# Kernel optimization log

Hardware: AMD Instinct MI355X
Metric: run time of the kernel (lower is better)

The kernel has to match this reference:

```python
import jax, jax.numpy as jnp
import numpy as np

N_EMBD = 1024
N_HEAD = 16
HEAD_DIM = N_EMBD // N_HEAD  # 64
KV_RANK = 256
Q_RANK = 512
ROPE_DIM = 32
B, T = 2, 2048
EPS = 1e-6


def _rope_tables(T, dim):
    inv_freq = 1.0 / (10000.0 ** (np.arange(0, dim, 2, dtype=np.float32) / dim))
    t = np.arange(T, dtype=np.float32)
    freqs = np.outer(t, inv_freq)            # [T, dim/2]
    emb = np.concatenate([freqs, freqs], -1)  # [T, dim]
    return jnp.asarray(np.cos(emb)), jnp.asarray(np.sin(emb))


def _apply_rope(x, cos, sin):
    # x: [B, H, T, D]; cos/sin: [T, D]
    d2 = x.shape[-1] // 2
    x1, x2 = x[..., :d2], x[..., d2:]
    rot = jnp.concatenate([-x2, x1], axis=-1)
    return x * cos[None, None, :, :] + rot * sin[None, None, :, :]


def setup_inputs() -> dict:
    key = jax.random.key(0)
    ks = jax.random.split(key, 10)
    def w(k, fan_in, fan_out):
        return jax.random.normal(k, (fan_in, fan_out), dtype=jnp.float32) * (fan_in ** -0.5)
    return {
        "x": jax.random.normal(ks[0], (B, T, N_EMBD), dtype=jnp.float32),
        "W_kv": w(ks[1], N_EMBD, KV_RANK),
        "g_kv": jnp.ones((KV_RANK,), dtype=jnp.float32),
        "W_kdec": w(ks[2], KV_RANK, N_HEAD * HEAD_DIM),
        "W_vdec": w(ks[3], KV_RANK, N_HEAD * HEAD_DIM),
        "W_q": w(ks[4], N_EMBD, Q_RANK),
        "W_qdec": w(ks[5], Q_RANK, N_HEAD * HEAD_DIM),
        "W_krope": w(ks[6], N_EMBD, N_HEAD * ROPE_DIM),
        "W_qrope": w(ks[7], Q_RANK, N_HEAD * ROPE_DIM),
        "W_o": w(ks[8], N_HEAD * HEAD_DIM, N_EMBD),
    }


def reference(x, W_kv, g_kv, W_kdec, W_vdec, W_q, W_qdec, W_krope, W_qrope, W_o):
    Bx, Tx, C = x.shape
    # low-rank compression
    kv_c = x @ W_kv                                    # [B,T,R_kv]
    kv_c = kv_c * jax.lax.rsqrt(jnp.mean(kv_c * kv_c, axis=-1, keepdims=True) + EPS) * g_kv
    q_c = x @ W_q                                       # [B,T,R_q]
    # decompress to per-head content / rope parts -> [B,H,T,D]
    def heads(y, d):
        return y.reshape(Bx, Tx, N_HEAD, d).transpose(0, 2, 1, 3)
    k_content = heads(kv_c @ W_kdec, HEAD_DIM)
    v = heads(kv_c @ W_vdec, HEAD_DIM)
    q_content = heads(q_c @ W_qdec, HEAD_DIM)
    k_rope = heads(x @ W_krope, ROPE_DIM)
    q_rope = heads(q_c @ W_qrope, ROPE_DIM)
    cos, sin = _rope_tables(Tx, ROPE_DIM)
    q_rope = _apply_rope(q_rope, cos, sin)
    k_rope = _apply_rope(k_rope, cos, sin)
    q = jnp.concatenate([q_content, q_rope], axis=-1)   # [B,H,T,D+Dr]
    k = jnp.concatenate([k_content, k_rope], axis=-1)
    scale = 1.0 / jnp.sqrt(jnp.float32(q.shape[-1]))
    scores = jnp.einsum('bhqd,bhkd->bhqk', q, k) * scale  # [B,H,T,T]
    causal = jnp.tril(jnp.ones((Tx, Tx), dtype=bool))
    scores = jnp.where(causal[None, None], scores, jnp.float32(-jnp.inf))
    attn = jax.nn.softmax(scores, axis=-1)
    out = jnp.einsum('bhqk,bhkd->bhqd', attn, v)          # [B,H,T,D]
    out = out.transpose(0, 2, 1, 3).reshape(Bx, Tx, N_HEAD * HEAD_DIM)
    return out @ W_o
```

## Files before the change

### kernel.cpp

```cpp
#include <hip/hip_runtime.h>
#include <hip/hip_bf16.h>
#include <math.h>

#define Bz 2
#define Tz 2048
#define Cz 1024
#define Hz 16
#define Dz 64
#define Rz 32
#define KVR 256
#define QR 512
#define DQK 96
#define Mz (Bz*Tz)
#define BHT (Bz*Hz*Tz)
#define QK_SCALE 0.10206207261596577f
#define QK_SCALE2 0.14724538519399733f
#define THR2 11.541560327111707f

typedef __attribute__((ext_vector_type(8))) short short8;
typedef __attribute__((ext_vector_type(4))) float f32x4;
typedef __attribute__((ext_vector_type(4))) unsigned short ushort4v;

__device__ __forceinline__ unsigned short f2bf(float f) {
    union { float f; unsigned u; } un; un.f = f;
    unsigned r = un.u + 0x7FFF + ((un.u >> 16) & 1);
    return (unsigned short)(r >> 16);
}

__device__ __forceinline__ void gload_lds16(const void* g, void* l) {
    __builtin_amdgcn_global_load_lds(
        (const __attribute__((address_space(1))) unsigned int*)g,
        (__attribute__((address_space(3))) unsigned int*)l, 16, 0, 0);
}

__global__ __launch_bounds__(256) void conv_f32_bf16(const float* __restrict__ in,
                                                     unsigned short* __restrict__ out,
                                                     int n)
{
    int i = (blockIdx.x * 256 + threadIdx.x) * 4;
    if (i >= n) return;
    float4 v = *(const float4*)&in[i];
    ushort4v o = { f2bf(v.x), f2bf(v.y), f2bf(v.z), f2bf(v.w) };
    *(ushort4v*)&out[i] = o;
}

struct TDesc8 {
    const float* src[8];
    unsigned short* dst[8];
    int K[8], N[8];
    int tile0[9];
};

__global__ __launch_bounds__(256) void transpose_all(TDesc8 p)
{
    __shared__ float ts[32][33];
    int t = blockIdx.x;
    int wi = 0;
    #pragma unroll
    for (int i = 0; i < 7; i++) if (t >= p.tile0[i + 1]) wi = i + 1;
    int lt = t - p.tile0[wi];
    int K = p.K[wi], N = p.N[wi];
    int kT = K >> 5;
    int k0 = (lt % kT) * 32, n0 = (lt / kT) * 32;
    const float* in = p.src[wi];
    unsigned short* out = p.dst[wi];

    int tid = threadIdx.x;
    int r = tid >> 5, cc = tid & 31;
    #pragma unroll
    for (int l = 0; l < 4; l++)
        ts[r + l * 8][cc] = in[(size_t)(k0 + r + l * 8) * N + n0 + cc];
    __syncthreads();
    #pragma unroll
    for (int l = 0; l < 4; l++)
        out[(size_t)(n0 + r + l * 8) * K + k0 + cc] = f2bf(ts[cc][r + l * 8]);
}

template<int EMODE>
__global__ __launch_bounds__(64) void gemm1w(
    const unsigned short* __restrict__ A, const unsigned short* __restrict__ Wt,
    void* __restrict__ O0, void* __restrict__ O1, void* __restrict__ O2,
    int K, float scale)
{
    __shared__ __attribute__((aligned(16))) unsigned short As[64 * 64];
    __shared__ __attribute__((aligned(16))) unsigned short Bs[64 * 64];

    const int lane = threadIdx.x;
    const int c = lane & 15, g = lane >> 4;
    const int m0 = blockIdx.x * 64, n0 = blockIdx.y * 64;
    const int rl = lane >> 3, c8 = lane & 7;

    f32x4 acc[4][4] = {};

    auto stage = [&](int k0) {
        if (EMODE == 4) {
            int h = k0 >> 6;
            #pragma unroll
            for (int i = 0; i < 8; i++) {
                int m = m0 + i * 8 + rl;
                int b = m >> 11, t = m & (Tz - 1);
                gload_lds16(&A[(((size_t)b * Hz + h) * Tz + t) * 64 + c8 * 8],
                            &As[(i * 64 + lane) * 8]);
            }
        } else {
            #pragma unroll
            for (int i = 0; i < 8; i++)
                gload_lds16(&A[(size_t)(m0 + i * 8 + rl) * K + k0 + c8 * 8],
                            &As[(i * 64 + lane) * 8]);
        }
        #pragma unroll
        for (int i = 0; i < 8; i++)
            gload_lds16(&Wt[(size_t)(n0 + i * 8 + rl) * K + k0 + c8 * 8],
                        &Bs[(i * 64 + lane) * 8]);
    };

    stage(0);

    for (int k0 = 0; k0 < K; k0 += 64) {
        asm volatile("s_waitcnt vmcnt(0)" ::: "memory");
        __builtin_amdgcn_sched_barrier(0);

        short8 af[2][4], bfr[2][4];
        #pragma unroll
        for (int ks = 0; ks < 2; ks++) {
            #pragma unroll
            for (int mq = 0; mq < 4; mq++)
                af[ks][mq] = *(const short8*)&As[(mq * 16 + c) * 64 + ks * 32 + g * 8];
            #pragma unroll
            for (int nt = 0; nt < 4; nt++)
                bfr[ks][nt] = *(const short8*)&Bs[(nt * 16 + c) * 64 + ks * 32 + g * 8];
        }
        asm volatile("s_waitcnt lgkmcnt(0)" ::: "memory");
        __builtin_amdgcn_sched_barrier(0);

        if (k0 + 64 < K) stage(k0 + 64);

        __builtin_amdgcn_s_setprio(1);
        #pragma unroll
        for (int ks = 0; ks < 2; ks++)
            #pragma unroll
            for (int mq = 0; mq < 4; mq++)
                #pragma unroll
                for (int nt = 0; nt < 4; nt++)
                    acc[mq][nt] = __builtin_amdgcn_mfma_f32_16x16x32_bf16(
                        af[ks][mq], bfr[ks][nt], acc[mq][nt], 0, 0, 0);
        __builtin_amdgcn_s_setprio(0);
    }

    #pragma unroll
    for (int mq = 0; mq < 4; mq++) {
        #pragma unroll
        for (int r = 0; r < 4; r++) {
            int m = m0 + mq * 16 + g * 4 + r;
            int b = m >> 11, t = m & (Tz - 1);

            if (EMODE == 1) {
                if (n0 < 256) {
                    #pragma unroll
                    for (int nt = 0; nt < 4; nt++)
                        ((float*)O0)[(size_t)m * 256 + n0 + nt * 16 + c] = acc[mq][nt][r];
                } else if (n0 < 768) {
                    #pragma unroll
                    for (int nt = 0; nt < 4; nt++)
                        ((unsigned short*)O1)[(size_t)m * 512 + (n0 - 256) + nt * 16 + c] =
                            f2bf(acc[mq][nt][r]);
                } else {
                    float inv = __expf(-(float)c * 0.5756462732485114f);
                    float ang = (float)t * inv;
                    float cs = cosf(ang), sn = sinf(ang);
                    #pragma unroll
                    for (int np = 0; np < 4; np += 2) {
                        float v0 = acc[mq][np][r];
                        float v1 = acc[mq][np + 1][r];
                        int col0 = (n0 - 768) + np * 16;
                        int h = col0 >> 5;
                        size_t base = (((size_t)b * Hz + h) * Tz + t) * DQK + 64;
                        ((unsigned short*)O2)[base + c]      = f2bf(v0 * cs - v1 * sn);
                        ((unsigned short*)O2)[base + c + 16] = f2bf(v1 * cs + v0 * sn);
                    }
                }
            } else if (EMODE == 2) {
                if (n0 < 1024) {
                    #pragma unroll
                    for (int nt = 0; nt < 4; nt++) {
                        int n = n0 + nt * 16 + c;
                        int h = n >> 6, dd = n & 63;
                        ((unsigned short*)O0)[(((size_t)b * Hz + h) * Tz + t) * DQK + dd] =
                            f2bf(acc[mq][nt][r] * scale);
                    }
                } else {
                    float inv = __expf(-(float)c * 0.5756462732485114f);
                    float ang = (float)t * inv;
                    float cs = cosf(ang), sn = sinf(ang);
                    #pragma unroll
                    for (int np = 0; np < 4; np += 2) {
                        float v0 = acc[mq][np][r] * scale;
                        float v1 = acc[mq][np + 1][r] * scale;
                        int col0 = (n0 - 1024) + np * 16;
                        int h = col0 >> 5;
                        size_t base = (((size_t)b * Hz + h) * Tz + t) * DQK + 64;
                        ((unsigned short*)O0)[base + c]      = f2bf(v0 * cs - v1 * sn);
                        ((unsigned short*)O0)[base + c + 16] = f2bf(v1 * cs + v0 * sn);
                    }
                }
            } else if (EMODE == 3) {
                if (n0 < 1024) {
                    #pragma unroll
                    for (int nt = 0; nt < 4; nt++) {
                        int n = n0 + nt * 16 + c;
                        int h = n >> 6, dd = n & 63;
                        ((unsigned short*)O0)[(((size_t)b * Hz + h) * Tz + t) * DQK + dd] =
                            f2bf(acc[mq][nt][r]);
                    }
                } else {
                    #pragma unroll
                    for (int nt = 0; nt < 4; nt++) {
                        int n = (n0 - 1024) + nt * 16 + c;
                        int h = n >> 6, dd = n & 63;
                        ((unsigned short*)O1)[(((size_t)b * Hz + h) * 64 + dd) * Tz + t] =
                            f2bf(acc[mq][nt][r]);
                    }
                }
            } else {
                #pragma unroll
                for (int nt = 0; nt < 4; nt++)
                    ((float*)O0)[(size_t)m * 1024 + n0 + nt * 16 + c] = acc[mq][nt][r];
            }
        }
    }
}

__global__ __launch_bounds__(256) void rmsnorm_k(const float* __restrict__ kv,
                                                 const float* __restrict__ g,
                                                 unsigned short* __restrict__ outb)
{
    int row = blockIdx.x * 4 + (threadIdx.x >> 6);
    int lane = threadIdx.x & 63;
    const float* p = kv + (size_t)row * 256;
    float v[4];
    float ss = 0.f;
    #pragma unroll
    for (int i = 0; i < 4; i++) { v[i] = p[lane + i * 64]; ss += v[i] * v[i]; }
    #pragma unroll
    for (int o = 32; o > 0; o >>= 1) ss += __shfl_xor(ss, o);
    float r = rsqrtf(ss * (1.f / 256.f) + 1e-6f);
    #pragma unroll
    for (int i = 0; i < 4; i++)
        outb[(size_t)row * 256 + lane + i * 64] = f2bf(v[i] * r * g[lane + i * 64]);
}

#define PSTR 72

__global__ __launch_bounds__(256, 3) void attn_mfma(
    const unsigned short* __restrict__ q,
    const unsigned short* __restrict__ k,
    const unsigned short* __restrict__ vt,
    unsigned short* __restrict__ o)
{
    __shared__ __attribute__((aligned(16))) unsigned short Ks[64 * 96];
    __shared__ __attribute__((aligned(16))) unsigned short Ps[4][16 * PSTR];

    int tid = threadIdx.x;
    int lane = tid & 63;
    int w = tid >> 6;
    int c = lane & 15, g = lane >> 4;

    int s = blockIdx.x;
    int bh = s & 31;
    int j = s >> 5;
    int qt = (j < 16) ? (31 - j) : (j - 16);
    int q0 = qt * 64;
    int ntiles = qt + 1;

    const unsigned short* qb = q + (size_t)bh * Tz * DQK;
    const unsigned short* kb = k + (size_t)bh * Tz * DQK;
    const unsigned short* vb = vt + (size_t)bh * 64 * Tz;
    unsigned short* ps = &Ps[w][0];

    int soff[3], sidx[3];
    #pragma unroll
    for (int i = 0; i < 3; i++) {
        int id2 = tid + i * 256;
        int srow = id2 / 12, sc8 = id2 % 12;
        soff[i] = srow * DQK + sc8 * 8;
        sidx[i] = (srow * 96 + sc8 * 8) ^ ((srow & 7) << 3);
    }

    short8 qf[3];
    {
        const unsigned short* qrow = qb + (size_t)(q0 + w * 16 + c) * DQK;
        #pragma unroll
        for (int kc = 0; kc < 3; kc++)
            qf[kc] = *(const short8*)(qrow + kc * 32 + g * 8);
    }

    short8 kreg[3];
    #pragma unroll
    for (int i = 0; i < 3; i++)
        kreg[i] = *(const short8*)&kb[soff[i]];
    #pragma unroll
    for (int i = 0; i < 3; i++)
        *(short8*)&Ks[sidx[i]] = kreg[i];
    __syncthreads();

    f32x4 oacc[4] = {};
    float mrun = -1e30f, lrun = 0.f;

    for (int t = 0; t < ntiles; t++) {
        int kt0 = t * 64;
        bool more = (t + 1) < ntiles;

        if (more) {
            #pragma unroll
            for (int i = 0; i < 3; i++)
                kreg[i] = *(const short8*)&kb[(size_t)(kt0 + 64) * DQK + soff[i]];
        }
        short8 vf[2][4];
        #pragma unroll
        for (int kc2 = 0; kc2 < 2; kc2++)
            #pragma unroll
            for (int nt = 0; nt < 4; nt++)
                vf[kc2][nt] = *(const short8*)&vb[(size_t)(nt * 16 + c) * Tz + kt0 + kc2 * 32 + g * 8];

        f32x4 sacc[4] = {};
        __builtin_amdgcn_s_setprio(1);
        #pragma unroll
        for (int kc = 0; kc < 3; kc++) {
            #pragma unroll
            for (int nt = 0; nt < 4; nt++) {
                short8 kf = *(const short8*)&Ks[((nt * 16 + c) * 96 + kc * 32 + g * 8) ^ ((c & 7) << 3)];
                sacc[nt] = __builtin_amdgcn_mfma_f32_16x16x32_bf16(kf, qf[kc], sacc[nt], 0, 0, 0);
            }
        }
        __builtin_amdgcn_s_setprio(0);

        __syncthreads();
        if (more) {
            #pragma unroll
            for (int i = 0; i < 3; i++)
                *(short8*)&Ks[sidx[i]] = kreg[i];
        }

        if (kt0 == q0) {
            #pragma unroll
            for (int nt = 0; nt < 4; nt++)
                #pragma unroll
                for (int r = 0; r < 4; r++)
                    if (nt * 16 + g * 4 + r > w * 16 + c)
                        sacc[nt][r] = -1e30f;
        }

        float pm = sacc[0][0];
        #pragma unroll
        for (int nt = 0; nt < 4; nt++)
            #pragma unroll
            for (int r = 0; r < 4; r++)
                pm = fmaxf(pm, sacc[nt][r]);
        pm = fmaxf(pm, __shfl_xor(pm, 16));
        pm = fmaxf(pm, __shfl_xor(pm, 32));

        bool need = pm > mrun + THR2;
        if (__ballot(need)) {
            float mn = fmaxf(mrun, pm);
            float sc = exp2f(mrun - mn);
            mrun = mn;
            float rs = 0.f;
            #pragma unroll
            for (int nt = 0; nt < 4; nt++)
                #pragma unroll
                for (int r = 0; r < 4; r++) {
                    sacc[nt][r] = exp2f(sacc[nt][r] - mrun);
                    rs += sacc[nt][r];
                }
            rs += __shfl_xor(rs, 16);
            rs += __shfl_xor(rs, 32);
            lrun = lrun * sc + rs;
            float scr[4];
            #pragma unroll
            for (int r = 0; r < 4; r++) scr[r] = __shfl(sc, g * 4 + r);
            #pragma unroll
            for (int nt = 0; nt < 4; nt++)
                #pragma unroll
                for (int r = 0; r < 4; r++)
                    oacc[nt][r] *= scr[r];
        } else {
            float rs = 0.f;
            #pragma unroll
            for (int nt = 0; nt < 4; nt++)
                #pragma unroll
                for (int r = 0; r < 4; r++) {
                    sacc[nt][r] = exp2f(sacc[nt][r] - mrun);
                    rs += sacc[nt][r];
                }
            rs += __shfl_xor(rs, 16);
            rs += __shfl_xor(rs, 32);
            lrun += rs;
        }

        #pragma unroll
        for (int nt = 0; nt < 4; nt++)
            #pragma unroll
            for (int rp = 0; rp < 2; rp++) {
                unsigned w32;
                asm("v_cvt_pk_bf16_f32 %0, %1, %2"
                    : "=v"(w32) : "v"(sacc[nt][2 * rp]), "v"(sacc[nt][2 * rp + 1]));
                *(unsigned*)&ps[c * PSTR + nt * 16 + g * 4 + 2 * rp] = w32;
            }
        __builtin_amdgcn_wave_barrier();

        __builtin_amdgcn_s_setprio(1);
        #pragma unroll
        for (int kc2 = 0; kc2 < 2; kc2++) {
            short8 pf = *(const short8*)&ps[c * PSTR + kc2 * 32 + g * 8];
            #pragma unroll
            for (int nt = 0; nt < 4; nt++)
                oacc[nt] = __builtin_amdgcn_mfma_f32_16x16x32_bf16(pf, vf[kc2][nt], oacc[nt], 0, 0, 0);
        }
        __builtin_amdgcn_s_setprio(0);
        __builtin_amdgcn_wave_barrier();

        __syncthreads();
    }

    float lr[4];
    #pragma unroll
    for (int r = 0; r < 4; r++) lr[r] = __shfl(lrun, g * 4 + r);
    #pragma unroll
    for (int nt = 0; nt < 4; nt++)
        #pragma unroll
        for (int r = 0; r < 4; r++)
            o[((size_t)bh * Tz + q0 + w * 16 + g * 4 + r) * 64 + nt * 16 + c] =
                f2bf(oacc[nt][r] / lr[r]);
}

extern "C" void kernel_launch(void* const* d_in, const int* in_sizes, int n_in,
                              void* d_out, int out_size, void* d_ws, size_t ws_size,
                              hipStream_t stream)
{
    const float* x       = (const float*)d_in[0];
    const float* W_kv    = (const float*)d_in[1];
    const float* g_kv    = (const float*)d_in[2];
    const float* W_kdec  = (const float*)d_in[3];
    const float* W_vdec  = (const float*)d_in[4];
    const float* W_q     = (const float*)d_in[5];
    const float* W_qdec  = (const float*)d_in[6];
    const float* W_krope = (const float*)d_in[7];
    const float* W_qrope = (const float*)d_in[8];
    const float* W_o     = (const float*)d_in[9];
    float* out = (float*)d_out;

    float* kv_f32 = (float*)d_ws;
    unsigned short* us = (unsigned short*)(kv_f32 + (size_t)Mz * KVR);
    unsigned short* x_bf  = us;               us += (size_t)Mz * Cz;
    unsigned short* kv_bf = us;               us += (size_t)Mz * KVR;
    unsigned short* qc_bf = us;               us += (size_t)Mz * QR;
    unsigned short* qbb   = us;               us += (size_t)BHT * DQK;
    unsigned short* kbb   = us;               us += (size_t)BHT * DQK;
    unsigned short* vtb   = us;               us += (size_t)BHT * 64;
    unsigned short* ob    = us;               us += (size_t)BHT * 64;
    unsigned short* wc1 = us;                 us += (size_t)1280 * Cz;
    unsigned short* wc2 = us;                 us += (size_t)1536 * QR;
    unsigned short* wc3 = us;                 us += (size_t)2048 * KVR;
    unsigned short* woT = us;                 us += (size_t)Cz * Cz;

    dim3 blk(256);

    conv_f32_bf16<<<dim3((Mz*Cz)/1024), blk, 0, stream>>>(x, x_bf, Mz*Cz);

    TDesc8 td;
    const float* tsrc[8] = {W_kv, W_q, W_krope, W_qdec, W_qrope, W_kdec, W_vdec, W_o};
    unsigned short* tdst[8] = {
        wc1, wc1 + (size_t)256 * Cz, wc1 + (size_t)768 * Cz,
        wc2, wc2 + (size_t)1024 * QR,
        wc3, wc3 + (size_t)1024 * KVR,
        woT };
    int tK[8] = {Cz, Cz, Cz, QR, QR, KVR, KVR, Cz};
    int tN[8] = {KVR, QR, Hz*Rz, Hz*Dz, Hz*Rz, Hz*Dz, Hz*Dz, Cz};
    int cum = 0;
    td.tile0[0] = 0;
    for (int i = 0; i < 8; i++) {
        td.src[i] = tsrc[i]; td.dst[i] = tdst[i]; td.K[i] = tK[i]; td.N[i] = tN[i];
        cum += (tK[i] / 32) * (tN[i] / 32);
        td.tile0[i + 1] = cum;
    }
    transpose_all<<<dim3(cum), blk, 0, stream>>>(td);

    gemm1w<1><<<dim3(Mz/64, 1280/64), dim3(64), 0, stream>>>(
        x_bf, wc1, kv_f32, qc_bf, kbb, Cz, 1.f);
    rmsnorm_k<<<dim3(Mz/4), blk, 0, stream>>>(kv_f32, g_kv, kv_bf);
    gemm1w<2><<<dim3(Mz/64, 1536/64), dim3(64), 0, stream>>>(
        qc_bf, wc2, qbb, nullptr, nullptr, QR, QK_SCALE2);
    gemm1w<3><<<dim3(Mz/64, 2048/64), dim3(64), 0, stream>>>(
        kv_bf, wc3, kbb, vtb, nullptr, KVR, 1.f);
    attn_mfma<<<dim3(1024), blk, 0, stream>>>(qbb, kbb, vtb, ob);
    gemm1w<4><<<dim3(Mz/64, Cz/64), dim3(64), 0, stream>>>(
        ob, woT, out, nullptr, nullptr, Cz, 1.f);
}
```

Measured before the change: 170.8 us.

## Split attention KV range across two blocks with merge kernel, fuse q/kv decoder GEMMs

```diff
diff --git a/kernel.cpp b/kernel.cpp
--- a/kernel.cpp
+++ b/kernel.cpp
@@ -25,6 +25,9 @@
     union { float f; unsigned u; } un; un.f = f;
     unsigned r = un.u + 0x7FFF + ((un.u >> 16) & 1);
     return (unsigned short)(r >> 16);
+}
+__device__ __forceinline__ float bf2f(unsigned short h) {
+    union { unsigned u; float f; } un; un.u = ((unsigned)h) << 16; return un.f;
 }
 
 __device__ __forceinline__ void gload_lds16(const void* g, void* l) {
@@ -179,14 +182,95 @@
                         ((unsigned short*)O2)[base + c + 16] = f2bf(v1 * cs + v0 * sn);
                     }
                 }
-            } else if (EMODE == 2) {
+            } else {
+                #pragma unroll
+                for (int nt = 0; nt < 4; nt++)
+                    ((float*)O0)[(size_t)m * 1024 + n0 + nt * 16 + c] = acc[mq][nt][r];
+            }
+        }
+    }
+}
+
+__global__ __launch_bounds__(64) void gemm1w23(
+    const unsigned short* __restrict__ A2, const unsigned short* __restrict__ W2,
+    unsigned short* __restrict__ qbb,
+    const unsigned short* __restrict__ A3, const unsigned short* __restrict__ W3,
+    unsigned short* __restrict__ kbb, unsigned short* __restrict__ vtb)
+{
+    const bool is2 = blockIdx.y < 24;
+    const unsigned short* A  = is2 ? A2 : A3;
+    const unsigned short* Wt = is2 ? W2 : W3;
+    const int K = is2 ? QR : KVR;
+    const int n0 = (is2 ? blockIdx.y : (blockIdx.y - 24)) * 64;
+
+    __shared__ __attribute__((aligned(16))) unsigned short As[64 * 64];
+    __shared__ __attribute__((aligned(16))) unsigned short Bs[64 * 64];
+
+    const int lane = threadIdx.x;
+    const int c = lane & 15, g = lane >> 4;
+    const int m0 = blockIdx.x * 64;
+    const int rl = lane >> 3, c8 = lane & 7;
+
+    f32x4 acc[4][4] = {};
+
+    auto stage = [&](int k0) {
+        #pragma unroll
+        for (int i = 0; i < 8; i++)
+            gload_lds16(&A[(size_t)(m0 + i * 8 + rl) * K + k0 + c8 * 8],
+                        &As[(i * 64 + lane) * 8]);
+        #pragma unroll
+        for (int i = 0; i < 8; i++)
+            gload_lds16(&Wt[(size_t)(n0 + i * 8 + rl) * K + k0 + c8 * 8],
+                        &Bs[(i * 64 + lane) * 8]);
+    };
+
+    stage(0);
+
+    for (int k0 = 0; k0 < K; k0 += 64) {
+        asm volatile("s_waitcnt vmcnt(0)" ::: "memory");
+        __builtin_amdgcn_sched_barrier(0);
+
+        short8 af[2][4], bfr[2][4];
+        #pragma unroll
+        for (int ks = 0; ks < 2; ks++) {
+            #pragma unroll
+            for (int mq = 0; mq < 4; mq++)
+                af[ks][mq] = *(const short8*)&As[(mq * 16 + c) * 64 + ks * 32 + g * 8];
+            #pragma unroll
+            for (int nt = 0; nt < 4; nt++)
+                bfr[ks][nt] = *(const short8*)&Bs[(nt * 16 + c) * 64 + ks * 32 + g * 8];
+        }
+        asm volatile("s_waitcnt lgkmcnt(0)" ::: "memory");
+        __builtin_amdgcn_sched_barrier(0);
+
+        if (k0 + 64 < K) stage(k0 + 64);
+
+        __builtin_amdgcn_s_setprio(1);
+        #pragma unroll
+        for (int ks = 0; ks < 2; ks++)
+            #pragma unroll
+            for (int mq = 0; mq < 4; mq++)
+                #pragma unroll
+                for (int nt = 0; nt < 4; nt++)
+                    acc[mq][nt] = __builtin_amdgcn_mfma_f32_16x16x32_bf16(
+                        af[ks][mq], bfr[ks][nt], acc[mq][nt], 0, 0, 0);
+        __builtin_amdgcn_s_setprio(0);
+    }
+
+    #pragma unroll
+    for (int mq = 0; mq < 4; mq++) {
+        #pragma unroll
+        for (int r = 0; r < 4; r++) {
+            int m = m0 + mq * 16 + g * 4 + r;
+            int b = m >> 11, t = m & (Tz - 1);
+            if (is2) {
                 if (n0 < 1024) {
                     #pragma unroll
                     for (int nt = 0; nt < 4; nt++) {
                         int n = n0 + nt * 16 + c;
                         int h = n >> 6, dd = n & 63;
-                        ((unsigned short*)O0)[(((size_t)b * Hz + h) * Tz + t) * DQK + dd] =
-                            f2bf(acc[mq][nt][r] * scale);
+                        ((unsigned short*)qbb)[(((size_t)b * Hz + h) * Tz + t) * DQK + dd] =
+                            f2bf(acc[mq][nt][r] * QK_SCALE2);
                     }
                 } else {
                     float inv = __expf(-(float)c * 0.5756462732485114f);
@@ -194,37 +278,31 @@
                     float cs = cosf(ang), sn = sinf(ang);
                     #pragma unroll
                     for (int np = 0; np < 4; np += 2) {
-                        float v0 = acc[mq][np][r] * scale;
-                        float v1 = acc[mq][np + 1][r] * scale;
+                        float v0 = acc[mq][np][r] * QK_SCALE2;
+                        float v1 = acc[mq][np + 1][r] * QK_SCALE2;
                         int col0 = (n0 - 1024) + np * 16;
                         int h = col0 >> 5;
                         size_t base = (((size_t)b * Hz + h) * Tz + t) * DQK + 64;
-                        ((unsigned short*)O0)[base + c]      = f2bf(v0 * cs - v1 * sn);
-                        ((unsigned short*)O0)[base + c + 16] = f2bf(v1 * cs + v0 * sn);
+                        qbb[base + c]      = f2bf(v0 * cs - v1 * sn);
+                        qbb[base + c + 16] = f2bf(v1 * cs + v0 * sn);
                     }
                 }
-            } else if (EMODE == 3) {
+            } else {
                 if (n0 < 1024) {
                     #pragma unroll
                     for (int nt = 0; nt < 4; nt++) {
                         int n = n0 + nt * 16 + c;
                         int h = n >> 6, dd = n & 63;
-                        ((unsigned short*)O0)[(((size_t)b * Hz + h) * Tz + t) * DQK + dd] =
-                            f2bf(acc[mq][nt][r]);
+                        kbb[(((size_t)b * Hz + h) * Tz + t) * DQK + dd] = f2bf(acc[mq][nt][r]);
                     }
                 } else {
                     #pragma unroll
                     for (int nt = 0; nt < 4; nt++) {
                         int n = (n0 - 1024) + nt * 16 + c;
                         int h = n >> 6, dd = n & 63;
-                        ((unsigned short*)O1)[(((size_t)b * Hz + h) * 64 + dd) * Tz + t] =
-                            f2bf(acc[mq][nt][r]);
+                        vtb[(((size_t)b * Hz + h) * 64 + dd) * Tz + t] = f2bf(acc[mq][nt][r]);
                     }
                 }
-            } else {
-                #pragma unroll
-                for (int nt = 0; nt < 4; nt++)
-                    ((float*)O0)[(size_t)m * 1024 + n0 + nt * 16 + c] = acc[mq][nt][r];
             }
         }
     }
@@ -255,7 +333,8 @@
     const unsigned short* __restrict__ q,
     const unsigned short* __restrict__ k,
     const unsigned short* __restrict__ vt,
-    unsigned short* __restrict__ o)
+    unsigned short* __restrict__ opart,
+    float2* __restrict__ ml)
 {
     __shared__ __attribute__((aligned(16))) unsigned short Ks[64 * 96];
     __shared__ __attribute__((aligned(16))) unsigned short Ps[4][16 * PSTR];
@@ -265,12 +344,17 @@
     int w = tid >> 6;
     int c = lane & 15, g = lane >> 4;
 
-    int s = blockIdx.x;
+    int blk = blockIdx.x;
+    int half = blk & 1;
+    int s = blk >> 1;
     int bh = s & 31;
     int j = s >> 5;
     int qt = (j < 16) ? (31 - j) : (j - 16);
     int q0 = qt * 64;
     int ntiles = qt + 1;
+    int nlo = ntiles >> 1;
+    int tstart = half ? nlo : 0;
+    int tend   = half ? ntiles : nlo;
 
     const unsigned short* qb = q + (size_t)bh * Tz * DQK;
     const unsigned short* kb = k + (size_t)bh * Tz * DQK;
@@ -295,32 +379,40 @@
     }
 
     short8 kreg[3];
-    #pragma unroll
-    for (int i = 0; i < 3; i++)
-        kreg[i] = *(const short8*)&kb[soff[i]];
-    #pragma unroll
-    for (int i = 0; i < 3; i++)
-        *(short8*)&Ks[sidx[i]] = kreg[i];
+    {
+        size_t kix0 = (size_t)tstart * (64 * DQK);
+        #pragma unroll
+        for (int i = 0; i < 3; i++)
+            kreg[i] = *(const short8*)&kb[kix0 + soff[i]];
+        #pragma unroll
+        for (int i = 0; i < 3; i++)
+            *(short8*)&Ks[sidx[i]] = kreg[i];
+    }
     __syncthreads();
 
     f32x4 oacc[4] = {};
     float mrun = -1e30f, lrun = 0.f;
 
-    for (int t = 0; t < ntiles; t++) {
-        int kt0 = t * 64;
-        bool more = (t + 1) < ntiles;
+    size_t kpre = (size_t)(tstart + 1) * (64 * DQK);
+    size_t vix  = (size_t)c * Tz + g * 8 + (size_t)tstart * 64;
+
+    for (int t = tstart; t < tend; t++) {
+        bool more = (t + 1) < tend;
 
         if (more) {
             #pragma unroll
             for (int i = 0; i < 3; i++)
-                kreg[i] = *(const short8*)&kb[(size_t)(kt0 + 64) * DQK + soff[i]];
-        }
+                kreg[i] = *(const short8*)&kb[kpre + soff[i]];
+        }
+        kpre += 64 * DQK;
+
         short8 vf[2][4];
         #pragma unroll
         for (int kc2 = 0; kc2 < 2; kc2++)
             #pragma unroll
             for (int nt = 0; nt < 4; nt++)
-                vf[kc2][nt] = *(const short8*)&vb[(size_t)(nt * 16 + c) * Tz + kt0 + kc2 * 32 + g * 8];
+                vf[kc2][nt] = *(const short8*)&vb[vix + (size_t)nt * (16 * Tz) + kc2 * 32];
+        vix += 64;
 
         f32x4 sacc[4] = {};
         __builtin_amdgcn_s_setprio(1);
@@ -341,7 +433,7 @@
                 *(short8*)&Ks[sidx[i]] = kreg[i];
         }
 
-        if (kt0 == q0) {
+        if (t == ntiles - 1 && half) {
             #pragma unroll
             for (int nt = 0; nt < 4; nt++)
                 #pragma unroll
@@ -422,15 +514,29 @@
         __syncthreads();
     }
 
-    float lr[4];
-    #pragma unroll
-    for (int r = 0; r < 4; r++) lr[r] = __shfl(lrun, g * 4 + r);
+    size_t rowbase = (size_t)bh * Tz + q0 + w * 16;
+    if (g == 0)
+        ml[(size_t)half * BHT + rowbase + c] = make_float2(mrun, lrun);
     #pragma unroll
     for (int nt = 0; nt < 4; nt++)
         #pragma unroll
         for (int r = 0; r < 4; r++)
-            o[((size_t)bh * Tz + q0 + w * 16 + g * 4 + r) * 64 + nt * 16 + c] =
-                f2bf(oacc[nt][r] / lr[r]);
+            opart[((size_t)half * BHT + rowbase + g * 4 + r) * 64 + nt * 16 + c] =
+                f2bf(oacc[nt][r]);
+}
+
+__global__ __launch_bounds__(256) void attn_merge(
+    const unsigned short* __restrict__ opart, const float2* __restrict__ ml,
+    unsigned short* __restrict__ ob)
+{
+    size_t idx = (size_t)blockIdx.x * 256 + threadIdx.x;
+    size_t row = idx >> 6;
+    float2 a = ml[row], b = ml[BHT + row];
+    float m = fmaxf(a.x, b.x);
+    float s0 = exp2f(a.x - m), s1 = exp2f(b.x - m);
+    float l = a.y * s0 + b.y * s1;
+    float o0 = bf2f(opart[idx]), o1 = bf2f(opart[(size_t)BHT * 64 + idx]);
+    ob[idx] = f2bf((o0 * s0 + o1 * s1) / l);
 }
 
 extern "C" void kernel_launch(void* const* d_in, const int* in_sizes, int n_in,
@@ -462,6 +568,8 @@
     unsigned short* wc2 = us;                 us += (size_t)1536 * QR;
     unsigned short* wc3 = us;                 us += (size_t)2048 * KVR;
     unsigned short* woT = us;                 us += (size_t)Cz * Cz;
+    unsigned short* opart = us;               us += (size_t)2 * BHT * 64;
+    float2* mlbuf = (float2*)us;              us += (size_t)2 * BHT * 2;
 
     dim3 blk(256);
 
@@ -488,11 +596,10 @@
     gemm1w<1><<<dim3(Mz/64, 1280/64), dim3(64), 0, stream>>>(
         x_bf, wc1, kv_f32, qc_bf, kbb, Cz, 1.f);
     rmsnorm_k<<<dim3(Mz/4), blk, 0, stream>>>(kv_f32, g_kv, kv_bf);
-    gemm1w<2><<<dim3(Mz/64, 1536/64), dim3(64), 0, stream>>>(
-        qc_bf, wc2, qbb, nullptr, nullptr, QR, QK_SCALE2);
-    gemm1w<3><<<dim3(Mz/64, 2048/64), dim3(64), 0, stream>>>(
-        kv_bf, wc3, kbb, vtb, nullptr, KVR, 1.f);
-    attn_mfma<<<dim3(1024), blk, 0, stream>>>(qbb, kbb, vtb, ob);
+    gemm1w23<<<dim3(Mz/64, 56), dim3(64), 0, stream>>>(
+        qc_bf, wc2, qbb, kv_bf, wc3, kbb, vtb);
+    attn_mfma<<<dim3(2048), blk, 0, stream>>>(qbb, kbb, vtb, opart, mlbuf);
+    attn_merge<<<dim3((BHT * 64) / 256), blk, 0, stream>>>(opart, mlbuf, ob);
     gemm1w<4><<<dim3(Mz/64, Cz/64), dim3(64), 0, stream>>>(
         ob, woT, out, nullptr, nullptr, Cz, 1.f);
 }
```

Result: slower. 177.0 us (+3.6%).
